# Kernel optimization log

Hardware: AMD Instinct MI355X
Metric: run time of the kernel (lower is better)

Reference implementation:

```python
import jax, jax.numpy as jnp
import numpy as np

T_DEC = 60  # decoder steps, hard-coded in the original forward

def _conv1d(x, w, b):
    # x: [B, C_in, L], w: [C_out, C_in, K] -> [B, C_out, L-K+1] (valid conv)
    y = jax.lax.conv_general_dilated(x, w, window_strides=(1,), padding='VALID',
                                     dimension_numbers=('NCH', 'OIH', 'NCH'))
    return y + b[None, :, None]

def _lstm_cell(x, h, c, wih, whh, bih, bhh):
    # PyTorch LSTM cell, gate order i, f, g, o
    g = x @ wih.T + h @ whh.T + (bih + bhh)
    i, f, gg, o = jnp.split(g, 4, axis=-1)
    c = jax.nn.sigmoid(f) * c + jax.nn.sigmoid(i) * jnp.tanh(gg)
    h = jax.nn.sigmoid(o) * jnp.tanh(c)
    return h, c

def _lstm_seq(xs, wih, whh, bih, bhh, reverse=False):
    # xs: [B, T, D] -> [B, T, H], zero initial state (PyTorch default)
    B, H = xs.shape[0], whh.shape[1]
    xs_t = jnp.swapaxes(xs, 0, 1)
    if reverse:
        xs_t = xs_t[::-1]
    def step(carry, x):
        h, c = carry
        h, c = _lstm_cell(x, h, c, wih, whh, bih, bhh)
        return (h, c), h
    init = (jnp.zeros((B, H), xs.dtype), jnp.zeros((B, H), xs.dtype))
    _, hs = jax.lax.scan(step, init, xs_t)
    if reverse:
        hs = hs[::-1]
    return jnp.swapaxes(hs, 0, 1)

def setup_inputs():
    key = jax.random.key(0)
    B, L, D_in, H, D_out = 64, 4096, 64, 256, 128
    C1, C2, C3 = 8, 16, 32
    ks = jax.random.split(key, 32)
    it = iter(ks)
    def p(shape, scale=0.1):
        return jax.random.normal(next(it), shape, jnp.float32) * scale
    inp = {}
    inp['x'] = jax.random.normal(next(it), (B, L, D_in), jnp.float32)
    inp['conv_w1'] = p((C1, D_in, 4)); inp['conv_b1'] = p((C1,))
    inp['conv_w2'] = p((C2, C1, 8));  inp['conv_b2'] = p((C2,))
    inp['conv_w3'] = p((C3, C2, 16)); inp['conv_b3'] = p((C3,))
    inp['attn_w'] = p((H, C3)); inp['attn_b'] = p((H,))
    inp['dec1_wih'] = p((2, 4 * H, C3)); inp['dec1_whh'] = p((2, 4 * H, H))
    inp['dec1_bih'] = p((2, 4 * H));     inp['dec1_bhh'] = p((2, 4 * H))
    inp['dec2_wih0'] = p((2, 4 * H, 2 * H)); inp['dec2_whh0'] = p((2, 4 * H, H))
    inp['dec2_bih0'] = p((2, 4 * H));        inp['dec2_bhh0'] = p((2, 4 * H))
    inp['dec2_wih1'] = p((2, 4 * H, 2 * H)); inp['dec2_whh1'] = p((2, 4 * H, H))
    inp['dec2_bih1'] = p((2, 4 * H));        inp['dec2_bhh1'] = p((2, 4 * H))
    inp['out_w'] = p((D_out, 2 * H)); inp['out_b'] = p((D_out,))
    return inp

def reference(x, conv_w1, conv_b1, conv_w2, conv_b2, conv_w3, conv_b3,
              attn_w, attn_b, dec1_wih, dec1_whh, dec1_bih, dec1_bhh,
              dec2_wih0, dec2_whh0, dec2_bih0, dec2_bhh0,
              dec2_wih1, dec2_whh1, dec2_bih1, dec2_bhh1, out_w, out_b):
    # Eval mode: all dropouts are identity.
    h = jnp.swapaxes(x, 1, 2)  # [B, D_in, L]
    h = jax.nn.relu(_conv1d(h, conv_w1, conv_b1))
    h = jax.nn.relu(_conv1d(h, conv_w2, conv_b2))
    h = jax.nn.relu(_conv1d(h, conv_w3, conv_b3))
    enc = jnp.swapaxes(h, 1, 2)  # [B, Lp, 32], Lp = L - 25
    keys_t = jnp.einsum('blc,hc->bhl', enc, attn_w) + attn_b[None, :, None]  # [B, H, Lp]
    B, H = x.shape[0], attn_w.shape[0]

    def dec1(wih, whh, bih, bhh):
        def step(carry, _):
            hh, cc = carry
            align = jnp.einsum('bh,bhl->bl', hh, keys_t)   # attention scores over Lp
            a = jax.nn.softmax(align, axis=-1)
            ctx = jnp.einsum('bl,blc->bc', a, enc)         # context [B, 32]
            hh, cc = _lstm_cell(ctx, hh, cc, wih, whh, bih, bhh)
            return (hh, cc), hh
        init = (jnp.zeros((B, H), x.dtype), jnp.zeros((B, H), x.dtype))
        _, hs = jax.lax.scan(step, init, None, length=T_DEC)
        return jnp.swapaxes(hs, 0, 1)  # [B, 60, H]

    fwd = dec1(dec1_wih[0], dec1_whh[0], dec1_bih[0], dec1_bhh[0])
    # the bkwd branch writes step i into slot 60-i-1, i.e. time-reversed outputs
    bkwd = dec1(dec1_wih[1], dec1_whh[1], dec1_bih[1], dec1_bhh[1])[:, ::-1]
    d2in = jnp.concatenate([fwd, bkwd], axis=-1)  # [B, 60, 2H]
    l0 = jnp.concatenate([
        _lstm_seq(d2in, dec2_wih0[0], dec2_whh0[0], dec2_bih0[0], dec2_bhh0[0]),
        _lstm_seq(d2in, dec2_wih0[1], dec2_whh0[1], dec2_bih0[1], dec2_bhh0[1], reverse=True)], axis=-1)
    l1 = jnp.concatenate([
        _lstm_seq(l0, dec2_wih1[0], dec2_whh1[0], dec2_bih1[0], dec2_bhh1[0]),
        _lstm_seq(l0, dec2_wih1[1], dec2_whh1[1], dec2_bih1[1], dec2_bhh1[1], reverse=True)], axis=-1)
    return l1 @ out_w.T + out_b  # [B, 60, D_out]
```

## Files before the change

### kernel.cpp

```cpp
#include <hip/hip_runtime.h>

#define B_    64
#define L1C   4093
#define L2C   4086
#define L3C   4071
#define TDEC  60

static __device__ __forceinline__ float sigf(float x){ return 1.f/(1.f + __expf(-x)); }

typedef _Float16 h2_t __attribute__((ext_vector_type(2)));
union U2H { unsigned u; h2_t h; };

static __device__ __forceinline__ unsigned pkh2(float a, float b){
  U2H r; r.h[0] = (_Float16)a; r.h[1] = (_Float16)b; return r.u;
}
static __device__ __forceinline__ float dot2f(unsigned w, unsigned h, float acc){
  U2H a; a.u = w; U2H b; b.u = h;
#if __has_builtin(__builtin_amdgcn_fdot2)
  return __builtin_amdgcn_fdot2(a.h, b.h, acc, false);
#else
  acc = fmaf((float)a.h[0], (float)b.h[0], acc);
  acc = fmaf((float)a.h[1], (float)b.h[1], acc);
  return acc;
#endif
}

#define DOT8(g, wv, hv) \
  g = dot2f(wv.x, hv.x, g); g = dot2f(wv.y, hv.y, g); \
  g = dot2f(wv.z, hv.z, g); g = dot2f(wv.w, hv.w, g);

template<int CTRL>
static __device__ __forceinline__ float dppadd(float x){
  int y = __builtin_amdgcn_update_dpp(0, __float_as_int(x), CTRL, 0xf, 0xf, true);
  return x + __int_as_float(y);
}

template<int CIN,int COUT,int KW>
__global__ __launch_bounds__(256) void k_conv(
    const float* __restrict__ in, const float* __restrict__ w,
    const float* __restrict__ bias, float* __restrict__ outp,
    int Lin_, int Lout_)
{
  int g = blockIdx.x*256 + threadIdx.x;
  int bi = g / Lout_;
  int l  = g - bi*Lout_;
  if (bi >= B_) return;
  float acc[COUT];
#pragma unroll
  for (int o=0;o<COUT;o++) acc[o] = bias[o];
  const float* ip = in + ((size_t)bi*Lin_ + l)*CIN;
  for (int k=0;k<KW;k++){
#pragma unroll
    for (int i4=0;i4<CIN/4;i4++){
      float4 xv = *(const float4*)(ip + k*CIN + i4*4);
#pragma unroll
      for (int c=0;c<4;c++){
        float xs = (&xv.x)[c];
        int i = i4*4+c;
#pragma unroll
        for (int o=0;o<COUT;o++)
          acc[o] = fmaf(xs, w[(o*CIN + i)*KW + k], acc[o]);
      }
    }
  }
  float* op = outp + ((size_t)bi*Lout_ + l)*COUT;
#pragma unroll
  for (int o=0;o<COUT;o++) op[o] = fmaxf(acc[o],0.f);
}

__global__ __launch_bounds__(256) void k_conv3q(
    const float* __restrict__ in, const float* __restrict__ w,
    const float* __restrict__ bias, uint4* __restrict__ encq,
    float* __restrict__ encs, int Lin_, int Lout_)
{
  int g = blockIdx.x*256 + threadIdx.x;
  int bi = g / Lout_;
  int l  = g - bi*Lout_;
  if (bi >= B_) return;
  float acc[32];
#pragma unroll
  for (int o=0;o<32;o++) acc[o] = bias[o];
  const float* ip = in + ((size_t)bi*Lin_ + l)*16;
  for (int k=0;k<16;k++){
#pragma unroll
    for (int i4=0;i4<4;i4++){
      float4 xv = *(const float4*)(ip + k*16 + i4*4);
#pragma unroll
      for (int c=0;c<4;c++){
        float xs = (&xv.x)[c];
        int i = i4*4+c;
#pragma unroll
        for (int o=0;o<32;o++)
          acc[o] = fmaf(xs, w[(o*16 + i)*16 + k], acc[o]);
      }
    }
  }
  float mx = 0.f;
#pragma unroll
  for (int o=0;o<32;o++){ acc[o] = fmaxf(acc[o],0.f); mx = fmaxf(mx, acc[o]); }
  float scale = mx * (1.f/255.f);
  float inv = (mx > 0.f) ? (255.f/mx) : 0.f;
  unsigned qs[8];
#pragma unroll
  for (int q8=0;q8<8;q8++){
    unsigned q0 = (unsigned)(acc[q8*4+0]*inv + 0.5f);
    unsigned q1 = (unsigned)(acc[q8*4+1]*inv + 0.5f);
    unsigned q2 = (unsigned)(acc[q8*4+2]*inv + 0.5f);
    unsigned q3 = (unsigned)(acc[q8*4+3]*inv + 0.5f);
    qs[q8] = q0 | (q1<<8) | (q2<<16) | (q3<<24);
  }
  uint4* op = encq + ((size_t)bi*Lout_ + l)*2;
  op[0] = make_uint4(qs[0],qs[1],qs[2],qs[3]);
  op[1] = make_uint4(qs[4],qs[5],qs[6],qs[7]);
  encs[(size_t)bi*Lout_ + l] = scale;
}

__global__ __launch_bounds__(256) void k_packwh(
    const float* __restrict__ w, uint4* __restrict__ wT, int K)
{
  int gid = blockIdx.x*256 + threadIdx.x;
  int per = (K/8)*1024;
  int d = gid / per, rem = gid - d*per;
  int j8 = rem >> 10, row = rem & 1023;
  const float* src = w + ((size_t)d*1024 + row)*K + j8*8;
  float4 a = *(const float4*)src;
  float4 b = *(const float4*)(src+4);
  uint4 o;
  o.x = pkh2(a.x, a.y);
  o.y = pkh2(a.z, a.w);
  o.z = pkh2(b.x, b.y);
  o.w = pkh2(b.z, b.w);
  wT[gid] = o;
}

#define CVT8(r, qv) \
  r[0]=(float)( qv.x      & 255u); r[1]=(float)((qv.x>>8 ) & 255u); \
  r[2]=(float)((qv.x>>16) & 255u); r[3]=(float)((qv.x>>24)       ); \
  r[4]=(float)( qv.y      & 255u); r[5]=(float)((qv.y>>8 ) & 255u); \
  r[6]=(float)((qv.y>>16) & 255u); r[7]=(float)((qv.y>>24)       );

__global__ __launch_bounds__(1024) void k_dec1g(
    const uint4* __restrict__ encq,
    const float* __restrict__ encs,
    const float* __restrict__ attn_w,
    const uint4* __restrict__ wihT,
    const uint4* __restrict__ whhT,
    const float* __restrict__ bih, const float* __restrict__ bhh,
    float* __restrict__ d2in)
{
  int b = blockIdx.x, d = blockIdx.y, tid = threadIdx.x;
  int c = tid & 3, rb = tid >> 2;

  __shared__ __align__(16) uint2 encQ2[16384];
  __shared__ float sls[4096];
  __shared__ __align__(16) float hls[256];
  __shared__ __align__(16) unsigned h2pk[128];
  __shared__ __align__(16) unsigned ctxh[16];
  __shared__ float vl[32];
  __shared__ float maxenc[32];
  __shared__ float Msh;
  __shared__ float red[1024];
  __shared__ float scr[512];
  __shared__ float gls[1024];

  {
    const uint4* src = encq + (size_t)b*L3C*2;
    uint4* dst = (uint4*)encQ2;
    for (int i = tid; i < 8192; i += 1024)
      dst[i] = (i < L3C*2) ? src[i] : make_uint4(0,0,0,0);
    const float* ss = encs + (size_t)b*L3C;
    for (int i = tid; i < 4096; i += 1024)
      sls[i] = (i < L3C) ? ss[i] : 0.f;
  }
  if (tid < 256) hls[tid] = 0.f;
  if (tid < 128) h2pk[tid] = 0u;
  float creg = 0.f;
  float bsum = bih[(size_t)d*1024 + tid] + bhh[(size_t)d*1024 + tid];
  const uint4* whp = whhT + (size_t)d*32768;
  __syncthreads();

  {
    float mc[8];
#pragma unroll
    for (int j=0;j<8;j++) mc[j] = 0.f;
#pragma unroll
    for (int k=0;k<16;k++){
      int l = rb + 256*k;
      uint2 qv = encQ2[l*4 + c];
      float sl = sls[l];
      float r[8]; CVT8(r, qv)
#pragma unroll
      for (int j=0;j<8;j++) mc[j] = fmaxf(mc[j], r[j]*sl);
    }
#pragma unroll
    for (int off=4; off<=32; off<<=1){
#pragma unroll
      for (int j=0;j<8;j++) mc[j] = fmaxf(mc[j], __shfl_xor(mc[j], off));
    }
    int wid = tid >> 6;
    if ((tid&63) < 4){
#pragma unroll
      for (int j=0;j<8;j++) scr[wid*32 + c*8 + j] = mc[j];
    }
    __syncthreads();
    if (tid < 32){
      float mm = 0.f;
#pragma unroll
      for (int w=0;w<16;w++) mm = fmaxf(mm, scr[w*32 + tid]);
      maxenc[tid] = mm;
    }
    __syncthreads();
  }

  for (int t=0; t<TDEC; t++){
    {
      int cc = tid & 31, part = tid >> 5;
      const float* wp = attn_w + (size_t)(part*8)*32 + cc;
      float s = 0.f;
#pragma unroll
      for (int k=0;k<8;k++) s = fmaf(hls[part*8+k], wp[k*32], s);
      red[tid] = s;
    }
    __syncthreads();
    if (tid < 32){
      float v = 0.f;
#pragma unroll
      for (int q=0;q<32;q++) v += red[q*32 + tid];
      vl[tid] = v;
      float mt = maxenc[tid] * fmaxf(v, 0.f);
#pragma unroll
      for (int off=1; off<32; off<<=1) mt += __shfl_xor(mt, off);
      if (tid==0) Msh = mt;
    }
    __syncthreads();

    float vreg[8];
#pragma unroll
    for (int j=0;j<8;j++) vreg[j] = vl[c*8 + j];
    float M = Msh;
    float ssum = 0.f;
    float acc[8];
#pragma unroll
    for (int j=0;j<8;j++) acc[j] = 0.f;
    float g = bsum;
#pragma unroll 4
    for (int k=0;k<16;k++){
      uint4 wv0 = whp[(2*k  )*1024 + tid];
      uint4 wv1 = whp[(2*k+1)*1024 + tid];
      int l = rb + 256*k;
      uint2 qv = encQ2[l*4 + c];
      float sl = sls[l];
      float r[8]; CVT8(r, qv)
      float s = 0.f;
#pragma unroll
      for (int j=0;j<8;j++) s = fmaf(r[j], vreg[j], s);
      s = dppadd<0xB1>(s);
      s = dppadd<0x4E>(s);
      s *= sl;
      if (l >= L3C) s = -3.0e38f;
      float e = __expf(s - M);
      ssum += e;
      float em = e * sl;
#pragma unroll
      for (int j=0;j<8;j++) acc[j] = fmaf(em, r[j], acc[j]);
      uint4 hv0 = *(const uint4*)&h2pk[(2*k  )*4];
      uint4 hv1 = *(const uint4*)&h2pk[(2*k+1)*4];
      DOT8(g, wv0, hv0)
      DOT8(g, wv1, hv1)
    }
    ssum = dppadd<0x124>(ssum); ssum = dppadd<0x128>(ssum);
    ssum += __shfl_xor(ssum, 16); ssum += __shfl_xor(ssum, 32);
#pragma unroll
    for (int j=0;j<8;j++){
      acc[j] = dppadd<0x124>(acc[j]); acc[j] = dppadd<0x128>(acc[j]);
      acc[j] += __shfl_xor(acc[j], 16); acc[j] += __shfl_xor(acc[j], 32);
    }
    int wid = tid >> 6;
    if ((tid&63) < 4){
#pragma unroll
      for (int j=0;j<8;j++) scr[wid*32 + c*8 + j] = acc[j];
    }
    if ((tid&63)==0) red[wid] = ssum;
    __syncthreads();
    if (tid < 32){
      float S = 0.f, s2 = 0.f;
#pragma unroll
      for (int w=0;w<16;w++){ S += red[w]; s2 += scr[w*32 + tid]; }
      float cv = s2 / S;
      float co = __shfl_xor(cv, 1);
      if (!(tid&1)) ctxh[tid>>1] = pkh2(cv, co);
    }
    __syncthreads();

#pragma unroll
    for (int c8=0;c8<4;c8++){
      uint4 wv = wihT[(size_t)d*4096 + c8*1024 + tid];
      uint4 hv = *(const uint4*)&ctxh[c8*4];
      DOT8(g, wv, hv)
    }
    gls[tid] = g;
    __syncthreads();
    if (tid < 256){
      float ii = sigf(gls[tid]);
      float ff = sigf(gls[256+tid]);
      float gg = tanhf(gls[512+tid]);
      float oo = sigf(gls[768+tid]);
      creg = fmaf(ff, creg, ii*gg);
      float hn = oo * tanhf(creg);
      hls[tid] = hn;
      float ho = __shfl_xor(hn, 1);
      if (!(tid&1)) h2pk[tid>>1] = pkh2(hn, ho);
      int tout = d ? (59 - t) : t;
      d2in[((size_t)b*60 + tout)*512 + d*256 + tid] = hn;
    }
    __syncthreads();
  }
}

__global__ __launch_bounds__(256) void k_gemm(
    const float* __restrict__ A, const float* __restrict__ W,
    float* __restrict__ C, const float* __restrict__ b1, const float* __restrict__ b2,
    int K, int ldc, size_t sW, size_t sC, int sB)
{
  int m0 = blockIdx.x * 128, n0 = blockIdx.y * 128, z = blockIdx.z;
  const float* Wz = W + (size_t)z*sW;
  float* Cz = C + (size_t)z*sC;
  const float* b1z = b1 + (size_t)z*sB;
  const float* b2z = b2 ? (b2 + (size_t)z*sB) : nullptr;
  __shared__ __align__(16) float As[16][132];
  __shared__ __align__(16) float Bs[16][132];
  int tid = threadIdx.x;
  int tx = tid & 15, ty = tid >> 4;
  int r = tid >> 2, c4 = tid & 3;
  float acc[8][8] = {};
  for (int k0=0; k0<K; k0+=16){
#pragma unroll
    for (int h=0; h<2; h++){
      int rr = r + h*64;
      float4 av = *(const float4*)(A  + (size_t)(m0+rr)*K + k0 + c4*4);
      float4 bv = *(const float4*)(Wz + (size_t)(n0+rr)*K + k0 + c4*4);
      As[c4*4+0][rr]=av.x; As[c4*4+1][rr]=av.y; As[c4*4+2][rr]=av.z; As[c4*4+3][rr]=av.w;
      Bs[c4*4+0][rr]=bv.x; Bs[c4*4+1][rr]=bv.y; Bs[c4*4+2][rr]=bv.z; Bs[c4*4+3][rr]=bv.w;
    }
    __syncthreads();
#pragma unroll
    for (int kk=0; kk<16; kk++){
      float a[8], bb[8];
      *(float4*)&a[0]  = *(const float4*)&As[kk][ty*8];
      *(float4*)&a[4]  = *(const float4*)&As[kk][ty*8+4];
      *(float4*)&bb[0] = *(const float4*)&Bs[kk][tx*8];
      *(float4*)&bb[4] = *(const float4*)&Bs[kk][tx*8+4];
#pragma unroll
      for (int i=0;i<8;i++)
#pragma unroll
        for (int j=0;j<8;j++)
          acc[i][j] = fmaf(a[i], bb[j], acc[i][j]);
    }
    __syncthreads();
  }
  float bb1[8];
#pragma unroll
  for (int j=0;j<8;j++){
    int n = n0 + tx*8 + j;
    bb1[j] = b1z[n] + (b2z ? b2z[n] : 0.f);
  }
#pragma unroll
  for (int i=0;i<8;i++){
    int m = m0 + ty*8 + i;
    float o[8];
#pragma unroll
    for (int j=0;j<8;j++) o[j] = acc[i][j] + bb1[j];
    *(float4*)(Cz + (size_t)m*ldc + n0 + tx*8)     = *(const float4*)&o[0];
    *(float4*)(Cz + (size_t)m*ldc + n0 + tx*8 + 4) = *(const float4*)&o[4];
  }
}

__global__ __launch_bounds__(1024) void k_rec2(
    const float* __restrict__ xg,
    const uint4* __restrict__ wT,
    float* __restrict__ out)
{
  int b = blockIdx.x, d = blockIdx.y, tid = threadIdx.x;
  __shared__ __align__(16) unsigned h2pk[128];
  __shared__ float gls[1024];
  float c = 0.f;
  if (tid < 128) h2pk[tid] = 0u;
  const uint4* wp = wT + (size_t)d*32*1024;
  uint4 wpre[16];
#pragma unroll
  for (int j=0;j<16;j++) wpre[j] = wp[j*1024 + tid];
  const float* xp = xg + (((size_t)d*64 + b)*60)*1024;
  __syncthreads();
  for (int step=0; step<TDEC; step++){
    int t = d ? (TDEC-1-step) : step;
    float g = xp[(size_t)t*1024 + tid];
#pragma unroll
    for (int j8=0;j8<16;j8++){
      uint4 hv = *(const uint4*)&h2pk[j8*4];
      DOT8(g, wpre[j8], hv)
    }
#pragma unroll 4
    for (int j8=16;j8<32;j8++){
      uint4 wv = wp[j8*1024 + tid];
      uint4 hv = *(const uint4*)&h2pk[j8*4];
      DOT8(g, wv, hv)
    }
    gls[tid] = g;
    __syncthreads();
    if (tid < 256){
      float ii = sigf(gls[tid]);
      float ff = sigf(gls[256+tid]);
      float gg = tanhf(gls[512+tid]);
      float oo = sigf(gls[768+tid]);
      c = fmaf(ff, c, ii*gg);
      float hn = oo * tanhf(c);
      float ho = __shfl_xor(hn, 1);
      if (!(tid&1)) h2pk[tid>>1] = pkh2(hn, ho);
      out[((size_t)b*60 + t)*512 + d*256 + tid] = hn;
    }
    __syncthreads();
  }
}

extern "C" void kernel_launch(void* const* d_in, const int* in_sizes, int n_in,
                              void* d_out, int out_size, void* d_ws, size_t ws_size,
                              hipStream_t stream) {
  const float* x      = (const float*)d_in[0];
  const float* cw1    = (const float*)d_in[1];
  const float* cb1    = (const float*)d_in[2];
  const float* cw2    = (const float*)d_in[3];
  const float* cb2    = (const float*)d_in[4];
  const float* cw3    = (const float*)d_in[5];
  const float* cb3    = (const float*)d_in[6];
  const float* attn_w = (const float*)d_in[7];
  const float* d1_wih = (const float*)d_in[9];
  const float* d1_whh = (const float*)d_in[10];
  const float* d1_bih = (const float*)d_in[11];
  const float* d1_bhh = (const float*)d_in[12];
  const float* w2_ih0 = (const float*)d_in[13];
  const float* w2_hh0 = (const float*)d_in[14];
  const float* b2_ih0 = (const float*)d_in[15];
  const float* b2_hh0 = (const float*)d_in[16];
  const float* w2_ih1 = (const float*)d_in[17];
  const float* w2_hh1 = (const float*)d_in[18];
  const float* b2_ih1 = (const float*)d_in[19];
  const float* b2_hh1 = (const float*)d_in[20];
  const float* out_w  = (const float*)d_in[21];
  const float* out_b  = (const float*)d_in[22];

  char* ws = (char*)d_ws;
  size_t off = 0;
  uint4* encq = (uint4*)(ws + off);
  float* encs = (float*)(ws + off + 8338432);
  off += 16675840;
  size_t off_h1 = off;
  float* h1buf = (float*)(ws + off); off += 8382464;
  float* h2buf = (float*)(ws + off); off += 16736256;
  float* d2in  = (float*)(ws + off_h1);
  float* l0    = (float*)(ws + off_h1 + 7864320);
  float* l1    = (float*)(ws + off_h1 + 15728640);
  uint4* wT    = (uint4*)(ws + off_h1 + 23592960);
  float* xg    = (float*)(ws + off); off += 31457280;
  uint4* d1whhT = (uint4*)xg;
  uint4* d1wihT = (uint4*)((char*)xg + 1048576);
  (void)ws_size; (void)in_sizes; (void)n_in; (void)out_size;

  k_packwh<<<256,256,0,stream>>>(d1_whh, d1whhT, 256);
  k_packwh<<<32, 256,0,stream>>>(d1_wih, d1wihT, 32);

  int g1 = (B_*L1C + 255)/256;
  k_conv<64,8,4><<<g1,256,0,stream>>>(x, cw1, cb1, h1buf, 4096, L1C);
  int g2 = (B_*L2C + 255)/256;
  k_conv<8,16,8><<<g2,256,0,stream>>>(h1buf, cw2, cb2, h2buf, L1C, L2C);
  int g3 = (B_*L3C + 255)/256;
  k_conv3q<<<g3,256,0,stream>>>(h2buf, cw3, cb3, encq, encs, L2C, L3C);

  k_dec1g<<<dim3(64,2),1024,0,stream>>>(encq, encs, attn_w, d1wihT, d1whhT,
                                        d1_bih, d1_bhh, d2in);

  k_packwh<<<256,256,0,stream>>>(w2_hh0, wT, 256);
  k_gemm<<<dim3(30,8,2),256,0,stream>>>(d2in, w2_ih0, xg, b2_ih0, b2_hh0,
                                        512, 1024, (size_t)1024*512, (size_t)3840*1024, 1024);
  k_rec2<<<dim3(64,2),1024,0,stream>>>(xg, wT, l0);
  k_packwh<<<256,256,0,stream>>>(w2_hh1, wT, 256);
  k_gemm<<<dim3(30,8,2),256,0,stream>>>(l0, w2_ih1, xg, b2_ih1, b2_hh1,
                                        512, 1024, (size_t)1024*512, (size_t)3840*1024, 1024);
  k_rec2<<<dim3(64,2),1024,0,stream>>>(xg, wT, l1);
  k_gemm<<<dim3(30,1,1),256,0,stream>>>(l1, out_w, (float*)d_out, out_b, nullptr,
                                        512, 128, 0, 0, 0);
}
```

Measured before the change: 1.606 ms.

## Stage conv inputs in LDS and use packed FP32 FMA across kernels

The conv kernels now use a 2D grid (tile of 256 positions per batch row) and stage the input window into padded shared memory, so overlapping taps are read from LDS instead of repeated global loads. The conv, attention-decoder and GEMM inner loops switch to v_pk_fma_f32 through inline asm, with split accumulators that are summed at the end. The recurrent kernel also keeps 20 rather than 16 weight vectors resident in registers per thread. Risks include higher register pressure, lower occupancy, and small changes in float summation order.

```diff
diff --git a/kernel.cpp b/kernel.cpp
--- a/kernel.cpp
+++ b/kernel.cpp
@@ -10,6 +10,7 @@
 
 typedef _Float16 h2_t __attribute__((ext_vector_type(2)));
 union U2H { unsigned u; h2_t h; };
+typedef float f32x2 __attribute__((ext_vector_type(2)));
 
 static __device__ __forceinline__ unsigned pkh2(float a, float b){
   U2H r; r.h[0] = (_Float16)a; r.h[1] = (_Float16)b; return r.u;
@@ -24,6 +25,11 @@
   return acc;
 #endif
 }
+static __device__ __forceinline__ f32x2 pkfma(f32x2 a, f32x2 b, f32x2 c){
+  f32x2 d;
+  asm("v_pk_fma_f32 %0, %1, %2, %3" : "=v"(d) : "v"(a), "v"(b), "v"(c));
+  return d;
+}
 
 #define DOT8(g, wv, hv) \
   g = dot2f(wv.x, hv.x, g); g = dot2f(wv.y, hv.y, g); \
@@ -35,69 +41,84 @@
   return x + __int_as_float(y);
 }
 
-template<int CIN,int COUT,int KW>
-__global__ __launch_bounds__(256) void k_conv(
+template<int CIN,int COUT,int KW,int CINP>
+__global__ __launch_bounds__(256) void k_convL(
     const float* __restrict__ in, const float* __restrict__ w,
     const float* __restrict__ bias, float* __restrict__ outp,
     int Lin_, int Lout_)
 {
-  int g = blockIdx.x*256 + threadIdx.x;
-  int bi = g / Lout_;
-  int l  = g - bi*Lout_;
-  if (bi >= B_) return;
-  float acc[COUT];
-#pragma unroll
-  for (int o=0;o<COUT;o++) acc[o] = bias[o];
-  const float* ip = in + ((size_t)bi*Lin_ + l)*CIN;
+  __shared__ float xs[(256+KW-1)*CINP];
+  int bi = blockIdx.y, l0 = blockIdx.x*256, tid = threadIdx.x;
+  int nrow = min(256+KW-1, Lin_-l0);
+  const float* ip = in + ((size_t)bi*Lin_ + l0)*CIN;
+  for (int i = tid; i < nrow*(CIN/4); i += 256){
+    int rr = i/(CIN/4), cc = i - rr*(CIN/4);
+    float4 v = *(const float4*)(ip + rr*CIN + cc*4);
+    float* dst = &xs[rr*CINP + cc*4];
+    dst[0]=v.x; dst[1]=v.y; dst[2]=v.z; dst[3]=v.w;
+  }
+  __syncthreads();
+  int l = l0 + tid;
+  if (l >= Lout_) return;
+  f32x2 acc2[COUT];
+#pragma unroll
+  for (int o=0;o<COUT;o++){ acc2[o][0]=bias[o]; acc2[o][1]=0.f; }
   for (int k=0;k<KW;k++){
-#pragma unroll
-    for (int i4=0;i4<CIN/4;i4++){
-      float4 xv = *(const float4*)(ip + k*CIN + i4*4);
-#pragma unroll
-      for (int c=0;c<4;c++){
-        float xs = (&xv.x)[c];
-        int i = i4*4+c;
-#pragma unroll
-        for (int o=0;o<COUT;o++)
-          acc[o] = fmaf(xs, w[(o*CIN + i)*KW + k], acc[o]);
+    const float* xr = &xs[(tid+k)*CINP];
+#pragma unroll
+    for (int c2=0;c2<CIN/2;c2++){
+      f32x2 xv; xv[0]=xr[2*c2]; xv[1]=xr[2*c2+1];
+#pragma unroll
+      for (int o=0;o<COUT;o++){
+        f32x2 wv; wv[0]=w[(o*CIN + 2*c2)*KW + k]; wv[1]=w[(o*CIN + 2*c2+1)*KW + k];
+        acc2[o] = pkfma(xv, wv, acc2[o]);
       }
     }
   }
   float* op = outp + ((size_t)bi*Lout_ + l)*COUT;
 #pragma unroll
-  for (int o=0;o<COUT;o++) op[o] = fmaxf(acc[o],0.f);
-}
-
-__global__ __launch_bounds__(256) void k_conv3q(
+  for (int o=0;o<COUT;o++) op[o] = fmaxf(acc2[o][0]+acc2[o][1], 0.f);
+}
+
+__global__ __launch_bounds__(256) void k_conv3qL(
     const float* __restrict__ in, const float* __restrict__ w,
     const float* __restrict__ bias, uint4* __restrict__ encq,
     float* __restrict__ encs, int Lin_, int Lout_)
 {
-  int g = blockIdx.x*256 + threadIdx.x;
-  int bi = g / Lout_;
-  int l  = g - bi*Lout_;
-  if (bi >= B_) return;
-  float acc[32];
-#pragma unroll
-  for (int o=0;o<32;o++) acc[o] = bias[o];
-  const float* ip = in + ((size_t)bi*Lin_ + l)*16;
+  __shared__ float xs[(256+15)*17];
+  int bi = blockIdx.y, l0 = blockIdx.x*256, tid = threadIdx.x;
+  int nrow = min(256+15, Lin_-l0);
+  const float* ip = in + ((size_t)bi*Lin_ + l0)*16;
+  for (int i = tid; i < nrow*4; i += 256){
+    int rr = i>>2, cc = i&3;
+    float4 v = *(const float4*)(ip + rr*16 + cc*4);
+    float* dst = &xs[rr*17 + cc*4];
+    dst[0]=v.x; dst[1]=v.y; dst[2]=v.z; dst[3]=v.w;
+  }
+  __syncthreads();
+  int l = l0 + tid;
+  if (l >= Lout_) return;
+  f32x2 acc2[32];
+#pragma unroll
+  for (int o=0;o<32;o++){ acc2[o][0]=bias[o]; acc2[o][1]=0.f; }
   for (int k=0;k<16;k++){
-#pragma unroll
-    for (int i4=0;i4<4;i4++){
-      float4 xv = *(const float4*)(ip + k*16 + i4*4);
-#pragma unroll
-      for (int c=0;c<4;c++){
-        float xs = (&xv.x)[c];
-        int i = i4*4+c;
-#pragma unroll
-        for (int o=0;o<32;o++)
-          acc[o] = fmaf(xs, w[(o*16 + i)*16 + k], acc[o]);
+    const float* xr = &xs[(tid+k)*17];
+#pragma unroll
+    for (int c2=0;c2<8;c2++){
+      f32x2 xv; xv[0]=xr[2*c2]; xv[1]=xr[2*c2+1];
+#pragma unroll
+      for (int o=0;o<32;o++){
+        f32x2 wv; wv[0]=w[(o*16 + 2*c2)*16 + k]; wv[1]=w[(o*16 + 2*c2+1)*16 + k];
+        acc2[o] = pkfma(xv, wv, acc2[o]);
       }
     }
   }
-  float mx = 0.f;
-#pragma unroll
-  for (int o=0;o<32;o++){ acc[o] = fmaxf(acc[o],0.f); mx = fmaxf(mx, acc[o]); }
+  float acc[32]; float mx = 0.f;
+#pragma unroll
+  for (int o=0;o<32;o++){
+    float a = acc2[o][0] + acc2[o][1];
+    acc[o] = fmaxf(a, 0.f); mx = fmaxf(mx, acc[o]);
+  }
   float scale = mx * (1.f/255.f);
   float inv = (mx > 0.f) ? (255.f/mx) : 0.f;
   unsigned qs[8];
@@ -234,14 +255,14 @@
     }
     __syncthreads();
 
-    float vreg[8];
-#pragma unroll
-    for (int j=0;j<8;j++) vreg[j] = vl[c*8 + j];
+    f32x2 v2[4];
+#pragma unroll
+    for (int q=0;q<4;q++){ v2[q][0] = vl[c*8+2*q]; v2[q][1] = vl[c*8+2*q+1]; }
     float M = Msh;
     float ssum = 0.f;
-    float acc[8];
-#pragma unroll
-    for (int j=0;j<8;j++) acc[j] = 0.f;
+    f32x2 a2[4];
+#pragma unroll
+    for (int q=0;q<4;q++){ a2[q][0]=0.f; a2[q][1]=0.f; }
     float g = bsum;
 #pragma unroll 4
     for (int k=0;k<16;k++){
@@ -250,10 +271,15 @@
       int l = rb + 256*k;
       uint2 qv = encQ2[l*4 + c];
       float sl = sls[l];
-      float r[8]; CVT8(r, qv)
-      float s = 0.f;
-#pragma unroll
-      for (int j=0;j<8;j++) s = fmaf(r[j], vreg[j], s);
+      f32x2 r2[4];
+      r2[0][0]=(float)( qv.x      & 255u); r2[0][1]=(float)((qv.x>>8 ) & 255u);
+      r2[1][0]=(float)((qv.x>>16) & 255u); r2[1][1]=(float)((qv.x>>24)       );
+      r2[2][0]=(float)( qv.y      & 255u); r2[2][1]=(float)((qv.y>>8 ) & 255u);
+      r2[3][0]=(float)((qv.y>>16) & 255u); r2[3][1]=(float)((qv.y>>24)       );
+      f32x2 s2; s2[0]=0.f; s2[1]=0.f;
+#pragma unroll
+      for (int q=0;q<4;q++) s2 = pkfma(r2[q], v2[q], s2);
+      float s = s2[0] + s2[1];
       s = dppadd<0xB1>(s);
       s = dppadd<0x4E>(s);
       s *= sl;
@@ -261,13 +287,17 @@
       float e = __expf(s - M);
       ssum += e;
       float em = e * sl;
-#pragma unroll
-      for (int j=0;j<8;j++) acc[j] = fmaf(em, r[j], acc[j]);
+      f32x2 em2; em2[0]=em; em2[1]=em;
+#pragma unroll
+      for (int q=0;q<4;q++) a2[q] = pkfma(em2, r2[q], a2[q]);
       uint4 hv0 = *(const uint4*)&h2pk[(2*k  )*4];
       uint4 hv1 = *(const uint4*)&h2pk[(2*k+1)*4];
       DOT8(g, wv0, hv0)
       DOT8(g, wv1, hv1)
     }
+    float acc[8];
+#pragma unroll
+    for (int q=0;q<4;q++){ acc[2*q]=a2[q][0]; acc[2*q+1]=a2[q][1]; }
     ssum = dppadd<0x124>(ssum); ssum = dppadd<0x128>(ssum);
     ssum += __shfl_xor(ssum, 16); ssum += __shfl_xor(ssum, 32);
 #pragma unroll
@@ -332,7 +362,11 @@
   int tid = threadIdx.x;
   int tx = tid & 15, ty = tid >> 4;
   int r = tid >> 2, c4 = tid & 3;
-  float acc[8][8] = {};
+  f32x2 acc2[8][4];
+#pragma unroll
+  for (int i=0;i<8;i++)
+#pragma unroll
+    for (int q=0;q<4;q++){ acc2[i][q][0]=0.f; acc2[i][q][1]=0.f; }
   for (int k0=0; k0<K; k0+=16){
 #pragma unroll
     for (int h=0; h<2; h++){
@@ -345,16 +379,20 @@
     __syncthreads();
 #pragma unroll
     for (int kk=0; kk<16; kk++){
-      float a[8], bb[8];
+      float a[8]; f32x2 bb2[4];
       *(float4*)&a[0]  = *(const float4*)&As[kk][ty*8];
       *(float4*)&a[4]  = *(const float4*)&As[kk][ty*8+4];
-      *(float4*)&bb[0] = *(const float4*)&Bs[kk][tx*8];
-      *(float4*)&bb[4] = *(const float4*)&Bs[kk][tx*8+4];
-#pragma unroll
-      for (int i=0;i<8;i++)
-#pragma unroll
-        for (int j=0;j<8;j++)
-          acc[i][j] = fmaf(a[i], bb[j], acc[i][j]);
+      float4 b0 = *(const float4*)&Bs[kk][tx*8];
+      float4 b1v = *(const float4*)&Bs[kk][tx*8+4];
+      bb2[0][0]=b0.x;  bb2[0][1]=b0.y;  bb2[1][0]=b0.z;  bb2[1][1]=b0.w;
+      bb2[2][0]=b1v.x; bb2[2][1]=b1v.y; bb2[3][0]=b1v.z; bb2[3][1]=b1v.w;
+#pragma unroll
+      for (int i=0;i<8;i++){
+        f32x2 ad; ad[0]=a[i]; ad[1]=a[i];
+#pragma unroll
+        for (int q=0;q<4;q++)
+          acc2[i][q] = pkfma(ad, bb2[q], acc2[i][q]);
+      }
     }
     __syncthreads();
   }
@@ -369,7 +407,10 @@
     int m = m0 + ty*8 + i;
     float o[8];
 #pragma unroll
-    for (int j=0;j<8;j++) o[j] = acc[i][j] + bb1[j];
+    for (int q=0;q<4;q++){
+      o[2*q]   = acc2[i][q][0] + bb1[2*q];
+      o[2*q+1] = acc2[i][q][1] + bb1[2*q+1];
+    }
     *(float4*)(Cz + (size_t)m*ldc + n0 + tx*8)     = *(const float4*)&o[0];
     *(float4*)(Cz + (size_t)m*ldc + n0 + tx*8 + 4) = *(const float4*)&o[4];
   }
@@ -386,21 +427,21 @@
   float c = 0.f;
   if (tid < 128) h2pk[tid] = 0u;
   const uint4* wp = wT + (size_t)d*32*1024;
-  uint4 wpre[16];
-#pragma unroll
-  for (int j=0;j<16;j++) wpre[j] = wp[j*1024 + tid];
+  uint4 wpre[20];
+#pragma unroll
+  for (int j=0;j<20;j++) wpre[j] = wp[j*1024 + tid];
   const float* xp = xg + (((size_t)d*64 + b)*60)*1024;
   __syncthreads();
   for (int step=0; step<TDEC; step++){
     int t = d ? (TDEC-1-step) : step;
     float g = xp[(size_t)t*1024 + tid];
 #pragma unroll
-    for (int j8=0;j8<16;j8++){
+    for (int j8=0;j8<20;j8++){
       uint4 hv = *(const uint4*)&h2pk[j8*4];
       DOT8(g, wpre[j8], hv)
     }
 #pragma unroll 4
-    for (int j8=16;j8<32;j8++){
+    for (int j8=20;j8<32;j8++){
       uint4 wv = wp[j8*1024 + tid];
       uint4 hv = *(const uint4*)&h2pk[j8*4];
       DOT8(g, wv, hv)
@@ -468,12 +509,9 @@
   k_packwh<<<256,256,0,stream>>>(d1_whh, d1whhT, 256);
   k_packwh<<<32, 256,0,stream>>>(d1_wih, d1wihT, 32);
 
-  int g1 = (B_*L1C + 255)/256;
-  k_conv<64,8,4><<<g1,256,0,stream>>>(x, cw1, cb1, h1buf, 4096, L1C);
-  int g2 = (B_*L2C + 255)/256;
-  k_conv<8,16,8><<<g2,256,0,stream>>>(h1buf, cw2, cb2, h2buf, L1C, L2C);
-  int g3 = (B_*L3C + 255)/256;
-  k_conv3q<<<g3,256,0,stream>>>(h2buf, cw3, cb3, encq, encs, L2C, L3C);
+  k_convL<64,8,4,65><<<dim3(16,B_),256,0,stream>>>(x, cw1, cb1, h1buf, 4096, L1C);
+  k_convL<8,16,8,9><<<dim3(16,B_),256,0,stream>>>(h1buf, cw2, cb2, h2buf, L1C, L2C);
+  k_conv3qL<<<dim3(16,B_),256,0,stream>>>(h2buf, cw3, cb3, encq, encs, L2C, L3C);
 
   k_dec1g<<<dim3(64,2),1024,0,stream>>>(encq, encs, attn_w, d1wihT, d1whhT,
                                         d1_bih, d1_bhh, d2in);
```

After: 1.863 ms. 1.16x slower.
